# Optimization experiments

Measured on AMD Instinct MI355X. Metric: run time of the kernel, lower is better.

## Reference

```python
import jax, jax.numpy as jnp
import numpy as np

EPS = 1e-8  # torch cosine_similarity eps


def setup_inputs() -> dict:
    key = jax.random.key(0)
    ks = jax.random.split(key, 6)
    N, D, E, mask_dim = 50000, 128, 600000, 1
    x = jax.random.normal(ks[0], (N, D), dtype=jnp.float32)
    mask = jax.random.normal(ks[1], (N, mask_dim), dtype=jnp.float32)
    edge_index = jax.random.randint(ks[2], (2, E), 0, N, dtype=jnp.int64)
    # Linear(input_dim, input_dim) params (orthogonal-ish init not needed for math check)
    W = jax.random.normal(ks[3], (D, D), dtype=jnp.float32) / np.sqrt(D)
    b_lin = jax.random.normal(ks[4], (D,), dtype=jnp.float32) * 0.01
    alpha = jnp.float32(0.001)
    bias = jnp.ones((mask_dim,), dtype=jnp.float32) * -3.0
    return {"x": x, "mask": mask, "edge_index": edge_index,
            "W": W, "b_lin": b_lin, "alpha": alpha, "bias": bias}


def _forward(x, mask, W, b_lin, alpha, bias, edge_index, K=5):
    N = x.shape[0]
    # x_fn: Linear + Tanh
    h = jnp.tanh(x @ W.T + b_lin)                    # [N, D]
    row, col = edge_index[0], edge_index[1]
    hs, hd = h[row], h[col]                          # [E, D] gathers
    ns = jnp.maximum(jnp.linalg.norm(hs, axis=-1), EPS)
    nd = jnp.maximum(jnp.linalg.norm(hd, axis=-1), EPS)
    cos = jnp.sum(hs * hd, axis=-1) / (ns * nd)      # [E]
    edge_weights = jax.nn.relu(cos)

    # APPNP with PyG defaults: gcn_norm with self-loops (weight 1), sym norm
    loops = jnp.arange(N, dtype=row.dtype)
    r2 = jnp.concatenate([row, loops])
    c2 = jnp.concatenate([col, loops])
    w2 = jnp.concatenate([edge_weights, jnp.ones((N,), dtype=edge_weights.dtype)])
    deg = jax.ops.segment_sum(w2, c2, num_segments=N)
    dinv = jnp.where(deg > 0, deg ** -0.5, 0.0)
    norm = dinv[r2] * w2 * dinv[c2]                  # [E+N]

    h0 = jax.nn.relu(mask)                           # [N, 1]
    f = h0
    for _ in range(K):
        msg = norm[:, None] * f[r2]                  # gather + weight
        agg = jax.ops.segment_sum(msg, c2, num_segments=N)  # scatter-add to targets
        f = (1.0 - alpha) * agg + alpha * h0
    fill = jnp.tanh(f - jax.nn.softplus(bias))
    return fill, edge_weights


def reference(x, mask, edge_index, W, b_lin, alpha, bias):
    return _forward(x, mask, W, b_lin, alpha, bias, edge_index, K=5)
```

## Files before the change

### kernel.cpp

```cpp
#include <hip/hip_runtime.h>
#include <hip/hip_bf16.h>
#include <hip/hip_fp16.h>
#include <math.h>

typedef _Float16 half8 __attribute__((ext_vector_type(8)));
typedef float f32x4 __attribute__((ext_vector_type(4)));

__device__ __forceinline__ float tanh_fast(float v) {
  float e = __expf(v + v);
  return 1.0f - 2.0f * __builtin_amdgcn_rcpf(e + 1.0f);
}

__device__ __forceinline__ float dot8h(float4 a, float4 b) {
  const __half2* pa = (const __half2*)&a;
  const __half2* pb = (const __half2*)&b;
  float s = 0.0f;
#pragma unroll
  for (int i = 0; i < 4; ++i) {
    float2 fa = __half22float2(pa[i]);
    float2 fb = __half22float2(pb[i]);
    s = fmaf(fa.x, fb.x, s);
    s = fmaf(fa.y, fb.y, s);
  }
  return s;
}

__global__ void k_zero(uint4* __restrict__ p, int n4) {
  int i = blockIdx.x * 256 + threadIdx.x;
  if (i < n4) p[i] = make_uint4(0u, 0u, 0u, 0u);
}

__global__ __launch_bounds__(256) void k_front(
    const float* __restrict__ x, const float* __restrict__ W,
    const float* __restrict__ bl, const float* __restrict__ mask,
    const int* __restrict__ cols, __half* __restrict__ hn,
    int* __restrict__ cnt8, unsigned short* __restrict__ rank,
    float* __restrict__ h0, float* __restrict__ f_a, int N, int E, int nblk,
    int wstride, int ntiles) {
  __shared__ _Float16 wsh[128 * 128];
  const int tid = threadIdx.x;
  const int bid = blockIdx.x;
  const int wv = tid >> 6, lane = tid & 63;
  const int r = lane & 15;
  const int g = lane >> 4;

  int t0 = bid * 4 + wv;

  float4 xv[8];
  {
    const float4* xr = (const float4*)(x + (size_t)(t0 * 16 + r) * 128);
#pragma unroll
    for (int ks = 0; ks < 4; ++ks) {
      xv[ks * 2] = xr[ks * 8 + g * 2];
      xv[ks * 2 + 1] = xr[ks * 8 + g * 2 + 1];
    }
  }

  {
    float4 wa[8], wb[8];
#pragma unroll
    for (int k = 0; k < 8; ++k) {
      int i = tid + k * 256;
      const float4* wr = (const float4*)(W + (i >> 4) * 128 + (i & 15) * 8);
      wa[k] = wr[0];
      wb[k] = wr[1];
    }
#pragma unroll
    for (int k = 0; k < 8; ++k) {
      int i = tid + k * 256;
      int row = i >> 4, cc = i & 15;
      half8 h;
      h[0] = (_Float16)wa[k].x; h[1] = (_Float16)wa[k].y;
      h[2] = (_Float16)wa[k].z; h[3] = (_Float16)wa[k].w;
      h[4] = (_Float16)wb[k].x; h[5] = (_Float16)wb[k].y;
      h[6] = (_Float16)wb[k].z; h[7] = (_Float16)wb[k].w;
      *(half8*)((char*)wsh + row * 256 + ((cc * 16) ^ ((row & 7) << 4))) = h;
    }
  }
  __syncthreads();

  float bv[8];
#pragma unroll
  for (int c = 0; c < 8; ++c) bv[c] = bl[c * 16 + r];

  int t = t0;
#pragma unroll
  for (int it = 0; it < 2; ++it) {
    const int row0 = t * 16;
    half8 afrag[4];
#pragma unroll
    for (int ks = 0; ks < 4; ++ks) {
      float4 lo = xv[ks * 2], hi = xv[ks * 2 + 1];
      half8 a;
      a[0] = (_Float16)lo.x; a[1] = (_Float16)lo.y;
      a[2] = (_Float16)lo.z; a[3] = (_Float16)lo.w;
      a[4] = (_Float16)hi.x; a[5] = (_Float16)hi.y;
      a[6] = (_Float16)hi.z; a[7] = (_Float16)hi.w;
      afrag[ks] = a;
    }
    const int tn = t + wstride;
    const bool hasnext = (it == 0) && (tn < ntiles);
    if (hasnext) {
      const float4* xr = (const float4*)(x + (size_t)(tn * 16 + r) * 128);
#pragma unroll
      for (int ks = 0; ks < 4; ++ks) {
        xv[ks * 2] = xr[ks * 8 + g * 2];
        xv[ks * 2 + 1] = xr[ks * 8 + g * 2 + 1];
      }
    }
    f32x4 acc[8];
#pragma unroll
    for (int c = 0; c < 8; ++c) acc[c] = (f32x4){0.f, 0.f, 0.f, 0.f};
#pragma unroll
    for (int c = 0; c < 8; ++c) {
      const char* base = (const char*)wsh + (c * 16 + r) * 256;
      const int sw = ((c * 16 + r) & 7) << 4;
#pragma unroll
      for (int ks = 0; ks < 4; ++ks) {
        half8 b = *(const half8*)(base + ((ks * 64 + g * 16) ^ sw));
        acc[c] = __builtin_amdgcn_mfma_f32_16x16x32_f16(afrag[ks], b, acc[c],
                                                        0, 0, 0);
      }
    }
    float tt[8][4];
    float ss[4] = {0.f, 0.f, 0.f, 0.f};
#pragma unroll
    for (int c = 0; c < 8; ++c) {
#pragma unroll
      for (int j = 0; j < 4; ++j) {
        float tv = tanh_fast(acc[c][j] + bv[c]);
        tt[c][j] = tv;
        ss[j] = fmaf(tv, tv, ss[j]);
      }
    }
#pragma unroll
    for (int j = 0; j < 4; ++j) {
#pragma unroll
      for (int o = 8; o; o >>= 1) ss[j] += __shfl_xor(ss[j], o);
      ss[j] = 1.0f / fmaxf(sqrtf(ss[j]), 1e-8f);
    }
#pragma unroll
    for (int c = 0; c < 8; ++c)
#pragma unroll
      for (int j = 0; j < 4; ++j)
        hn[(size_t)(row0 + g * 4 + j) * 128 + c * 16 + r] =
            __float2half_rn(tt[c][j] * ss[j]);
    if (!hasnext) break;
    t = tn;
  }

  const int tg = bid * 256 + tid;
  const int NT = nblk * 256;
  for (int i = tg; i < N; i += NT) {
    float v = fmaxf(mask[i], 0.0f);
    h0[i] = v;
    f_a[i] = v;
  }
  for (int e = tg; e < E; e += NT) {
    int c = cols[e];
    int copy = (e >> 8) & 7;
    int rk = atomicAdd(cnt8 + copy * N + c, 1);
    rank[e] = (unsigned short)rk;
  }
}

__global__ __launch_bounds__(256) void k_scan_a(const int* __restrict__ cnt8,
                                                int* __restrict__ bsum,
                                                int N) {
  __shared__ int s[256];
  int i = blockIdx.x * 256 + threadIdx.x;
  int tot = 0;
  if (i < N) {
#pragma unroll
    for (int j = 0; j < 8; ++j) tot += cnt8[j * N + i];
  }
  s[threadIdx.x] = tot;
  __syncthreads();
  for (int d = 128; d; d >>= 1) {
    if (threadIdx.x < d) s[threadIdx.x] += s[threadIdx.x + d];
    __syncthreads();
  }
  if (threadIdx.x == 0) bsum[blockIdx.x] = s[0];
}

__global__ __launch_bounds__(256) void k_scan_bc(int* __restrict__ cnt8,
                                                 const int* __restrict__ bsum,
                                                 int* __restrict__ off, int N,
                                                 int E, int NCH) {
  __shared__ int bscan[2 * 256];
  __shared__ int cscan[2 * 256];
  const int t = threadIdx.x, bid = blockIdx.x;
  int bv = (t < NCH) ? bsum[t] : 0;
  bscan[t] = bv;
  __syncthreads();
  int a = 0;
  for (int d = 1; d < 256; d <<= 1) {
    int v2 = bscan[a * 256 + t];
    if (t >= d) v2 += bscan[a * 256 + t - d];
    bscan[(a ^ 1) * 256 + t] = v2;
    __syncthreads();
    a ^= 1;
  }
  int bpre = (bid > 0) ? bscan[a * 256 + bid - 1] : 0;
  int i = bid * 256 + t;
  int cj[8];
  int tot = 0;
  if (i < N) {
#pragma unroll
    for (int j = 0; j < 8; ++j) {
      cj[j] = cnt8[j * N + i];
      tot += cj[j];
    }
  }
  cscan[t] = tot;
  __syncthreads();
  int b2 = 0;
  for (int d = 1; d < 256; d <<= 1) {
    int v2 = cscan[b2 * 256 + t];
    if (t >= d) v2 += cscan[b2 * 256 + t - d];
    cscan[(b2 ^ 1) * 256 + t] = v2;
    __syncthreads();
    b2 ^= 1;
  }
  if (i < N) {
    int excl = cscan[b2 * 256 + t] - tot + bpre;
    off[i] = excl;
    int run = excl;
#pragma unroll
    for (int j = 0; j < 8; ++j) {
      cnt8[j * N + i] = run;
      run += cj[j];
    }
  }
  if (bid == 0 && t == 0) off[N] = E;
}

__global__ void k_build(const int* __restrict__ rows,
                        const int* __restrict__ cols,
                        const int* __restrict__ base8,
                        const unsigned short* __restrict__ rank,
                        unsigned* __restrict__ rec, int* __restrict__ perm,
                        int N, int E) {
  int e = blockIdx.x * 256 + threadIdx.x;
  if (e >= E) return;
  unsigned r = (unsigned)rows[e], c = (unsigned)cols[e];
  int copy = (e >> 8) & 7;
  int pos = base8[copy * N + (int)c] + (int)rank[e];
  rec[pos] = r | (c << 16);
  perm[e] = pos;
}

__global__ __launch_bounds__(256) void k_edge_cos(
    const __half* __restrict__ hn, const unsigned* __restrict__ rec,
    float* __restrict__ csr_w, unsigned short* __restrict__ src16, int E,
    int Q) {
  int t = blockIdx.x * 256 + threadIdx.x;
  int q = t >> 2, sub = t & 3;
  if (q >= Q) return;
  const int p0 = q, p1 = q + Q;
  const bool has1 = p1 < E;
  unsigned rc0 = rec[p0];
  unsigned rc1 = has1 ? rec[p1] : rc0;
  const float4* hr0 = (const float4*)(hn + (size_t)(rc0 & 0xffffu) * 128);
  const float4* hr1 = (const float4*)(hn + (size_t)(rc1 & 0xffffu) * 128);
  float4 r00 = hr0[sub], r01 = hr0[sub + 4], r02 = hr0[sub + 8],
         r03 = hr0[sub + 12];
  float4 r10 = hr1[sub], r11 = hr1[sub + 4], r12 = hr1[sub + 8],
         r13 = hr1[sub + 12];
  const float4* hc0 = (const float4*)(hn + (size_t)(rc0 >> 16) * 128);
  const float4* hc1 = (const float4*)(hn + (size_t)(rc1 >> 16) * 128);
  float d0 = dot8h(r00, hc0[sub]) + dot8h(r01, hc0[sub + 4]) +
             dot8h(r02, hc0[sub + 8]) + dot8h(r03, hc0[sub + 12]);
  float d1 = dot8h(r10, hc1[sub]) + dot8h(r11, hc1[sub + 4]) +
             dot8h(r12, hc1[sub + 8]) + dot8h(r13, hc1[sub + 12]);
  d0 += __shfl_xor(d0, 1);
  d0 += __shfl_xor(d0, 2);
  d1 += __shfl_xor(d1, 1);
  d1 += __shfl_xor(d1, 2);
  if (sub == 0) {
    csr_w[p0] = fmaxf(d0, 0.0f);
    src16[p0] = (unsigned short)(rc0 & 0xffffu);
    if (has1) {
      csr_w[p1] = fmaxf(d1, 0.0f);
      src16[p1] = (unsigned short)(rc1 & 0xffffu);
    }
  }
}

__global__ __launch_bounds__(256) void k_unperm_rsd(
    const float* __restrict__ csr_w, const int* __restrict__ perm,
    const int* __restrict__ off, float* __restrict__ ew,
    float* __restrict__ rsd, int N, int E) {
  int t = blockIdx.x * 256 + threadIdx.x;
  if (t < E) ew[t] = csr_w[perm[t]];
  int n = t >> 2, sub = t & 3;
  if (n < N) {
    int s0 = off[n], s1 = off[n + 1];
    float s = 0.0f;
    for (int i = s0 + sub; i < s1; i += 4) s += csr_w[i];
    s += __shfl_xor(s, 1);
    s += __shfl_xor(s, 2);
    if (sub == 0) rsd[n] = rsqrtf(1.0f + s);
  }
}

__global__ __launch_bounds__(256) void k_prop(
    const float* __restrict__ f_in, float* __restrict__ f_out,
    float* __restrict__ csr_w, const unsigned short* __restrict__ src16,
    const int* __restrict__ off, const float* __restrict__ h0,
    const float* __restrict__ rsd, const float* __restrict__ alpha_p,
    const float* __restrict__ bias_p, float* __restrict__ fill, int N,
    int mode) {
  int t = blockIdx.x * 256 + threadIdx.x;
  int n = t >> 2, sub = t & 3;
  if (n >= N) return;
  float rs_n = rsd[n];
  int s0 = off[n], s1 = off[n + 1];
  float part = 0.0f;
  if (mode & 1) {
    for (int i = s0 + sub; i < s1; i += 4) {
      int s = src16[i];
      float wn = csr_w[i] * rs_n * rsd[s];
      csr_w[i] = wn;
      part = fmaf(wn, f_in[s], part);
    }
  } else {
    for (int i = s0 + sub; i < s1; i += 4)
      part = fmaf(csr_w[i], f_in[src16[i]], part);
  }
  part += __shfl_xor(part, 1);
  part += __shfl_xor(part, 2);
  if (sub == 0) {
    float a = alpha_p[0];
    float agg = part + f_in[n] * rs_n * rs_n;
    float fn = (1.0f - a) * agg + a * h0[n];
    if (mode & 2) {
      float b = bias_p[0];
      float sp = (b > 20.0f) ? b : log1pf(expf(b));
      fill[n] = tanhf(fn - sp);
    } else {
      f_out[n] = fn;
    }
  }
}

extern "C" void kernel_launch(void* const* d_in, const int* in_sizes, int n_in,
                              void* d_out, int out_size, void* d_ws,
                              size_t ws_size, hipStream_t stream) {
  const float* x = (const float*)d_in[0];
  const float* mask = (const float*)d_in[1];
  const int* ei = (const int*)d_in[2];
  const float* W = (const float*)d_in[3];
  const float* bl = (const float*)d_in[4];
  const float* alpha = (const float*)d_in[5];
  const float* bias = (const float*)d_in[6];

  const int D = 128;
  const int N = in_sizes[0] / D;
  const int E = in_sizes[2] / 2;
  const int* rows = ei;
  const int* cols = ei + E;

  float* fill = (float*)d_out;
  float* ew = (float*)d_out + N;

  char* w = (char*)d_ws;
  size_t off_b = 0;
  auto alloc = [&](size_t bytes) -> void* {
    void* p = (void*)(w + off_b);
    off_b = (off_b + bytes + 255) & ~(size_t)255;
    return p;
  };
  __half* hn = (__half*)alloc((size_t)N * D * sizeof(__half));
  int* cnt8 = (int*)alloc((size_t)8 * N * sizeof(int));
  unsigned short* rank =
      (unsigned short*)alloc((size_t)E * sizeof(unsigned short));
  int* off = (int*)alloc((size_t)(N + 1) * sizeof(int));
  int* bsum = (int*)alloc(256 * sizeof(int));
  unsigned* rec = (unsigned*)alloc((size_t)E * sizeof(unsigned));
  int* perm = (int*)alloc((size_t)E * sizeof(int));
  float* csr_w = (float*)alloc((size_t)E * sizeof(float));
  unsigned short* src16 =
      (unsigned short*)alloc((size_t)E * sizeof(unsigned short));
  float* h0 = (float*)alloc((size_t)N * sizeof(float));
  float* f_a = (float*)alloc((size_t)N * sizeof(float));
  float* f_b = (float*)alloc((size_t)N * sizeof(float));
  float* rsd = (float*)alloc((size_t)N * sizeof(float));
  (void)ws_size;

  const int NCH = (N + 255) / 256;
  const int nb_E = (E + 255) / 256;
  const int NTILES = (N + 15) / 16;
  const int FRONT_BLOCKS = (NTILES + 7) / 8;
  const int WSTRIDE = FRONT_BLOCKS * 4;

  const int n4 = (8 * N + 3) / 4;
  k_zero<<<(n4 + 255) / 256, 256, 0, stream>>>((uint4*)cnt8, n4);
  k_front<<<FRONT_BLOCKS, 256, 0, stream>>>(x, W, bl, mask, cols, hn, cnt8,
                                            rank, h0, f_a, N, E, FRONT_BLOCKS,
                                            WSTRIDE, NTILES);
  k_scan_a<<<NCH, 256, 0, stream>>>(cnt8, bsum, N);
  k_scan_bc<<<NCH, 256, 0, stream>>>(cnt8, bsum, off, N, E, NCH);
  k_build<<<nb_E, 256, 0, stream>>>(rows, cols, cnt8, rank, rec, perm, N, E);
  const int Q = (E + 1) / 2;
  k_edge_cos<<<(Q * 4 + 255) / 256, 256, 0, stream>>>(hn, rec, csr_w, src16,
                                                      E, Q);
  k_unperm_rsd<<<nb_E, 256, 0, stream>>>(csr_w, perm, off, ew, rsd, N, E);
  const float* fi = f_a;
  float* fo = f_b;
  for (int it = 0; it < 5; ++it) {
    int mode = (it == 0 ? 1 : 0) | (it == 4 ? 2 : 0);
    k_prop<<<(N * 4 + 255) / 256, 256, 0, stream>>>(
        fi, fo, csr_w, src16, off, h0, rsd, alpha, bias, fill, N, mode);
    const float* tmp = fo;
    fo = (float*)fi;
    fi = tmp;
  }
}
```

Measured before the change: 118.3 us.

## Fuse five propagation launches into one cooperative kernel with grid syncs

After: 426.3 us. +260.3%, slower.

```diff
diff --git a/kernel.cpp b/kernel.cpp
--- a/kernel.cpp
+++ b/kernel.cpp
@@ -1,7 +1,10 @@
 #include <hip/hip_runtime.h>
 #include <hip/hip_bf16.h>
 #include <hip/hip_fp16.h>
+#include <hip/hip_cooperative_groups.h>
 #include <math.h>
+
+namespace cg = cooperative_groups;
 
 typedef _Float16 half8 __attribute__((ext_vector_type(8)));
 typedef float f32x4 __attribute__((ext_vector_type(4)));
@@ -304,43 +307,67 @@
   }
 }
 
-__global__ __launch_bounds__(256) void k_prop(
-    const float* __restrict__ f_in, float* __restrict__ f_out,
+__global__ __launch_bounds__(256) void k_prop_all(
+    float* __restrict__ f_a, float* __restrict__ f_b,
     float* __restrict__ csr_w, const unsigned short* __restrict__ src16,
     const int* __restrict__ off, const float* __restrict__ h0,
     const float* __restrict__ rsd, const float* __restrict__ alpha_p,
-    const float* __restrict__ bias_p, float* __restrict__ fill, int N,
-    int mode) {
-  int t = blockIdx.x * 256 + threadIdx.x;
-  int n = t >> 2, sub = t & 3;
-  if (n >= N) return;
-  float rs_n = rsd[n];
-  int s0 = off[n], s1 = off[n + 1];
-  float part = 0.0f;
-  if (mode & 1) {
+    const float* __restrict__ bias_p, float* __restrict__ fill, int N) {
+  cg::grid_group grid = cg::this_grid();
+  const int t = blockIdx.x * 256 + threadIdx.x;
+  const int n = t >> 2, sub = t & 3;
+  const bool active = n < N;
+  const float a = alpha_p[0];
+
+  float rs_n = 0.f, selfw = 0.f, h0v = 0.f;
+  int s0 = 0, s1 = 0, ispill = 0;
+  float w0 = 0.f, w1 = 0.f, w2 = 0.f, w3 = 0.f;
+  int sx0 = 0, sx1 = 0, sx2 = 0, sx3 = 0;
+
+  if (active) {
+    rs_n = rsd[n];
+    selfw = rs_n * rs_n;
+    h0v = h0[n];
+    s0 = off[n];
+    s1 = off[n + 1];
     for (int i = s0 + sub; i < s1; i += 4) {
       int s = src16[i];
-      float wn = csr_w[i] * rs_n * rsd[s];
-      csr_w[i] = wn;
-      part = fmaf(wn, f_in[s], part);
-    }
-  } else {
-    for (int i = s0 + sub; i < s1; i += 4)
-      part = fmaf(csr_w[i], f_in[src16[i]], part);
-  }
-  part += __shfl_xor(part, 1);
-  part += __shfl_xor(part, 2);
-  if (sub == 0) {
-    float a = alpha_p[0];
-    float agg = part + f_in[n] * rs_n * rs_n;
-    float fn = (1.0f - a) * agg + a * h0[n];
-    if (mode & 2) {
-      float b = bias_p[0];
-      float sp = (b > 20.0f) ? b : log1pf(expf(b));
-      fill[n] = tanhf(fn - sp);
-    } else {
-      f_out[n] = fn;
-    }
+      csr_w[i] *= rs_n * rsd[s];
+    }
+    const int i0 = s0 + sub;
+    if (i0 < s1)          { sx0 = src16[i0];      w0 = csr_w[i0]; }
+    if (i0 + 4 < s1)      { sx1 = src16[i0 + 4];  w1 = csr_w[i0 + 4]; }
+    if (i0 + 8 < s1)      { sx2 = src16[i0 + 8];  w2 = csr_w[i0 + 8]; }
+    if (i0 + 12 < s1)     { sx3 = src16[i0 + 12]; w3 = csr_w[i0 + 12]; }
+    ispill = i0 + 16;
+  }
+
+  const float bvl = bias_p[0];
+  const float sp = (bvl > 20.0f) ? bvl : log1pf(expf(bvl));
+
+#pragma unroll
+  for (int it = 0; it < 5; ++it) {
+    const float* fi = (it & 1) ? f_b : f_a;
+    float* fo = (it & 1) ? f_a : f_b;
+    if (active) {
+      float part = w0 * fi[sx0];
+      part = fmaf(w1, fi[sx1], part);
+      part = fmaf(w2, fi[sx2], part);
+      part = fmaf(w3, fi[sx3], part);
+      for (int i = ispill; i < s1; i += 4)
+        part = fmaf(csr_w[i], fi[src16[i]], part);
+      part += __shfl_xor(part, 1);
+      part += __shfl_xor(part, 2);
+      if (sub == 0) {
+        float agg = part + fi[n] * selfw;
+        float fn = (1.0f - a) * agg + a * h0v;
+        if (it == 4)
+          fill[n] = tanhf(fn - sp);
+        else
+          fo[n] = fn;
+      }
+    }
+    if (it < 4) grid.sync();
   }
 }
 
@@ -406,14 +433,22 @@
   k_edge_cos<<<(Q * 4 + 255) / 256, 256, 0, stream>>>(hn, rec, csr_w, src16,
                                                       E, Q);
   k_unperm_rsd<<<nb_E, 256, 0, stream>>>(csr_w, perm, off, ew, rsd, N, E);
-  const float* fi = f_a;
-  float* fo = f_b;
-  for (int it = 0; it < 5; ++it) {
-    int mode = (it == 0 ? 1 : 0) | (it == 4 ? 2 : 0);
-    k_prop<<<(N * 4 + 255) / 256, 256, 0, stream>>>(
-        fi, fo, csr_w, src16, off, h0, rsd, alpha, bias, fill, N, mode);
-    const float* tmp = fo;
-    fo = (float*)fi;
-    fi = tmp;
-  }
-}
+  {
+    const int PROP_BLOCKS = (N * 4 + 255) / 256;
+    float* f_a_p = f_a;
+    float* f_b_p = f_b;
+    float* csr_w_p = csr_w;
+    const unsigned short* src16_p = src16;
+    const int* off_p = off;
+    const float* h0_p = h0;
+    const float* rsd_p = rsd;
+    const float* alpha_p = alpha;
+    const float* bias_p = bias;
+    float* fill_p = fill;
+    int N_v = N;
+    void* args[] = {&f_a_p, &f_b_p, &csr_w_p, &src16_p, &off_p, &h0_p,
+                    &rsd_p, &alpha_p, &bias_p, &fill_p, &N_v};
+    hipLaunchCooperativeKernel((const void*)k_prop_all, dim3(PROP_BLOCKS),
+                               dim3(256), args, 0, stream);
+  }
+}
```
